# Performance work log

Measured on AMD Instinct MI355X. Metric: run time of the kernel, lower is better.

The kernel has to match this reference:

```python
import jax, jax.numpy as jnp
import numpy as np

MIN_EXP = 1    # log2(min_window=2)
MAX_EXP = 10   # log2(max_window=1024)
OUT_LEN = 16384  # reconstructed signal length L; encoded len = L*(1 - 2**-MAX_EXP)


def setup_inputs() -> dict:
    key = jax.random.key(0)
    k1, k2, k3 = jax.random.split(key, 3)
    B = 2048
    enc_len = OUT_LEN * (2 ** (1 - MIN_EXP)) - OUT_LEN // (2 ** MAX_EXP)  # 16368
    weights_len = 2 * (2 ** MAX_EXP) - 1  # 2047
    stdev = 1.0 / np.sqrt(weights_len)
    data = jax.random.normal(k1, (B, enc_len), dtype=jnp.float32)
    weights = jax.random.uniform(k2, (weights_len,), dtype=jnp.float32, minval=-stdev, maxval=stdev)
    bias = jax.random.uniform(k3, (MAX_EXP,), dtype=jnp.float32, minval=-stdev, maxval=stdev)
    return {"data": data, "weights": weights, "bias": bias}


def reference(data, weights, bias):
    """Transposed time-scale convolution: for each dyadic scale e (window w=2**e),
    the shared kernel weights[w-1:2w-1] is overlap-added (stride == window, so the
    windows tile the output exactly) scaled by that scale's coefficients, summed
    across scales, with a per-scale bias."""
    B = data.shape[0]
    out = jnp.zeros((B, OUT_LEN), dtype=data.dtype)
    offset = 0
    for e in range(MIN_EXP, MAX_EXP + 1):
        w = 2 ** e
        n = OUT_LEN // w                      # number of windows at this scale
        kern = weights[w - 1: 2 * w - 1]      # [w] kernel for this scale
        coeffs = data[:, offset: offset + n]  # [B, n]
        offset += n
        # transposed conv with stride = kernel size: outer product then tile
        contrib = (coeffs[:, :, None] * kern[None, None, :]).reshape(B, OUT_LEN)
        out = out + contrib + bias[e - 1]
    return out
```

## Files before the change

### kernel.cpp

```cpp
#include <hip/hip_runtime.h>
#include <hip/hip_bf16.h>

#define TSC_OUT_LEN 16384
#define TSC_ENC_LEN 16368

__global__ __launch_bounds__(256) void tsc_transpose_kernel(
    const float* __restrict__ data,
    const float* __restrict__ weights,
    const float* __restrict__ bias,
    float* __restrict__ out)
{
    __shared__ float wl[2048];
    const int tid = threadIdx.x;
    for (int i = tid; i < 2047; i += 256) wl[i + 1] = weights[i];
    if (tid == 0) wl[0] = 0.0f;
    __syncthreads();

    float bs = 0.0f;
#pragma unroll
    for (int i = 0; i < 10; ++i) bs += bias[i];

    const int b    = blockIdx.x >> 3;
    const int tile = (blockIdx.x & 7) << 11;
    const int j0   = tile + (tid << 3);
    const float* drow = data + (size_t)b * TSC_ENC_LEN;

    float acc[8];
#pragma unroll
    for (int k = 0; k < 8; ++k) acc[k] = bs;

    {
        const float4 d4 = *reinterpret_cast<const float4*>(drow + (j0 >> 1));
        const float w1 = wl[2], w2 = wl[3];
        acc[0] += d4.x * w1; acc[1] += d4.x * w2;
        acc[2] += d4.y * w1; acc[3] += d4.y * w2;
        acc[4] += d4.z * w1; acc[5] += d4.z * w2;
        acc[6] += d4.w * w1; acc[7] += d4.w * w2;
    }
    {
        const float2 d2 = *reinterpret_cast<const float2*>(drow + 8192 + (j0 >> 2));
        const float4 kv = *reinterpret_cast<const float4*>(&wl[4]);
        acc[0] += d2.x * kv.x; acc[1] += d2.x * kv.y;
        acc[2] += d2.x * kv.z; acc[3] += d2.x * kv.w;
        acc[4] += d2.y * kv.x; acc[5] += d2.y * kv.y;
        acc[6] += d2.y * kv.z; acc[7] += d2.y * kv.w;
    }
#pragma unroll
    for (int e = 3; e <= 10; ++e) {
        const int w   = 1 << e;
        const int off = TSC_OUT_LEN - (TSC_OUT_LEN >> (e - 1));
        const float c = drow[off + (j0 >> e)];
        const int  kb = w + (j0 & (w - 1));
        const float4 k0 = *reinterpret_cast<const float4*>(&wl[kb]);
        const float4 k1 = *reinterpret_cast<const float4*>(&wl[kb + 4]);
        acc[0] += c * k0.x; acc[1] += c * k0.y;
        acc[2] += c * k0.z; acc[3] += c * k0.w;
        acc[4] += c * k1.x; acc[5] += c * k1.y;
        acc[6] += c * k1.z; acc[7] += c * k1.w;
    }

    float4* o = reinterpret_cast<float4*>(out + (size_t)b * TSC_OUT_LEN + j0);
    o[0] = make_float4(acc[0], acc[1], acc[2], acc[3]);
    o[1] = make_float4(acc[4], acc[5], acc[6], acc[7]);
}

extern "C" void kernel_launch(void* const* d_in, const int* in_sizes, int n_in,
                              void* d_out, int out_size, void* d_ws, size_t ws_size,
                              hipStream_t stream) {
    const float* data    = (const float*)d_in[0];
    const float* weights = (const float*)d_in[1];
    const float* bias    = (const float*)d_in[2];
    float* out = (float*)d_out;

    const int B = in_sizes[0] / TSC_ENC_LEN;
    dim3 grid(B * 8);
    dim3 block(256);
    tsc_transpose_kernel<<<grid, block, 0, stream>>>(data, weights, bias, out);
}
```

Baseline: 238.9 us.

## Process eight rows per block with double-buffered loads and hoisted kernel weights

Each block now handles eight batch rows instead of one. Kernel weight slices are loaded from LDS into registers once per block, with the smallest scales broadcast via readfirstlane, and reused for every row. Loads for the next row are issued before the current row is computed, and outputs are written with nontemporal stores. This amortises the per-block LDS fill and bias reduction and overlaps memory latency, at the cost of more registers, a grid eight times smaller, and an assumption that B is divisible by eight.

```diff
diff --git a/kernel.cpp b/kernel.cpp
--- a/kernel.cpp
+++ b/kernel.cpp
@@ -1,8 +1,22 @@
 #include <hip/hip_runtime.h>
-#include <hip/hip_bf16.h>
 
 #define TSC_OUT_LEN 16384
 #define TSC_ENC_LEN 16368
+#define TSC_ROWS 8
+
+typedef float f32x4 __attribute__((ext_vector_type(4)));
+
+__device__ __forceinline__ float tsc_rfl(float x) {
+    return __uint_as_float(__builtin_amdgcn_readfirstlane(__float_as_uint(x)));
+}
+
+struct TscLd {
+    float4 d1;
+    float2 d2;
+    float  c3;
+    float  c4, c5, c6, c7, c8;
+    float  c9, c10;
+};
 
 __global__ __launch_bounds__(256) void tsc_transpose_kernel(
     const float* __restrict__ data,
@@ -13,55 +27,103 @@
     __shared__ float wl[2048];
     const int tid = threadIdx.x;
     for (int i = tid; i < 2047; i += 256) wl[i + 1] = weights[i];
-    if (tid == 0) wl[0] = 0.0f;
     __syncthreads();
+
+    const int tile = blockIdx.x & 7;
+    const int rg   = blockIdx.x >> 3;
+    const int j0   = (tile << 11) + (tid << 3);
 
     float bs = 0.0f;
 #pragma unroll
     for (int i = 0; i < 10; ++i) bs += bias[i];
 
-    const int b    = blockIdx.x >> 3;
-    const int tile = (blockIdx.x & 7) << 11;
-    const int j0   = tile + (tid << 3);
-    const float* drow = data + (size_t)b * TSC_ENC_LEN;
+    const float w1a = tsc_rfl(wl[2]), w1b = tsc_rfl(wl[3]);
+    const float w2a = tsc_rfl(wl[4]), w2b = tsc_rfl(wl[5]);
+    const float w2c = tsc_rfl(wl[6]), w2d = tsc_rfl(wl[7]);
+    float w3[8];
+#pragma unroll
+    for (int i = 0; i < 8; ++i) w3[i] = tsc_rfl(wl[8 + i]);
 
-    float acc[8];
+    float4 wa[7], wb[7];
 #pragma unroll
-    for (int k = 0; k < 8; ++k) acc[k] = bs;
-
-    {
-        const float4 d4 = *reinterpret_cast<const float4*>(drow + (j0 >> 1));
-        const float w1 = wl[2], w2 = wl[3];
-        acc[0] += d4.x * w1; acc[1] += d4.x * w2;
-        acc[2] += d4.y * w1; acc[3] += d4.y * w2;
-        acc[4] += d4.z * w1; acc[5] += d4.z * w2;
-        acc[6] += d4.w * w1; acc[7] += d4.w * w2;
-    }
-    {
-        const float2 d2 = *reinterpret_cast<const float2*>(drow + 8192 + (j0 >> 2));
-        const float4 kv = *reinterpret_cast<const float4*>(&wl[4]);
-        acc[0] += d2.x * kv.x; acc[1] += d2.x * kv.y;
-        acc[2] += d2.x * kv.z; acc[3] += d2.x * kv.w;
-        acc[4] += d2.y * kv.x; acc[5] += d2.y * kv.y;
-        acc[6] += d2.y * kv.z; acc[7] += d2.y * kv.w;
-    }
-#pragma unroll
-    for (int e = 3; e <= 10; ++e) {
-        const int w   = 1 << e;
-        const int off = TSC_OUT_LEN - (TSC_OUT_LEN >> (e - 1));
-        const float c = drow[off + (j0 >> e)];
-        const int  kb = w + (j0 & (w - 1));
-        const float4 k0 = *reinterpret_cast<const float4*>(&wl[kb]);
-        const float4 k1 = *reinterpret_cast<const float4*>(&wl[kb + 4]);
-        acc[0] += c * k0.x; acc[1] += c * k0.y;
-        acc[2] += c * k0.z; acc[3] += c * k0.w;
-        acc[4] += c * k1.x; acc[5] += c * k1.y;
-        acc[6] += c * k1.z; acc[7] += c * k1.w;
+    for (int e = 4; e <= 10; ++e) {
+        const int w  = 1 << e;
+        const int kb = w + (j0 & (w - 1));
+        wa[e - 4] = *reinterpret_cast<const float4*>(&wl[kb]);
+        wb[e - 4] = *reinterpret_cast<const float4*>(&wl[kb + 4]);
     }
 
-    float4* o = reinterpret_cast<float4*>(out + (size_t)b * TSC_OUT_LEN + j0);
-    o[0] = make_float4(acc[0], acc[1], acc[2], acc[3]);
-    o[1] = make_float4(acc[4], acc[5], acc[6], acc[7]);
+    const int i1 = (j0 >> 1);
+    const int i2 = 8192  + (j0 >> 2);
+    const int i3 = 12288 + (j0 >> 3);
+    const int i4 = 14336 + (j0 >> 4);
+    const int i5 = 15360 + (j0 >> 5);
+    const int i6 = 15872 + (j0 >> 6);
+    const int i7 = 16128 + (j0 >> 7);
+    const int i8 = 16256 + (j0 >> 8);
+    const int i9  = 16320 + __builtin_amdgcn_readfirstlane(j0 >> 9);
+    const int i10 = 16352 + __builtin_amdgcn_readfirstlane(j0 >> 10);
+
+    const float* drow = data + (size_t)rg * TSC_ROWS * TSC_ENC_LEN;
+    float*       orow = out  + (size_t)rg * TSC_ROWS * TSC_OUT_LEN + j0;
+
+    auto issue = [&](const float* dp, TscLd& L) {
+        L.d1  = *reinterpret_cast<const float4*>(dp + i1);
+        L.d2  = *reinterpret_cast<const float2*>(dp + i2);
+        L.c3  = dp[i3];
+        L.c4  = dp[i4];
+        L.c5  = dp[i5];
+        L.c6  = dp[i6];
+        L.c7  = dp[i7];
+        L.c8  = dp[i8];
+        L.c9  = dp[i9];
+        L.c10 = dp[i10];
+    };
+
+    auto compute_store = [&](const TscLd& L, float* op) {
+        float a0 = bs, a1 = bs, a2 = bs, a3 = bs;
+        float a4 = bs, a5 = bs, a6 = bs, a7 = bs;
+        a0 = fmaf(L.d1.x, w1a, a0); a1 = fmaf(L.d1.x, w1b, a1);
+        a2 = fmaf(L.d1.y, w1a, a2); a3 = fmaf(L.d1.y, w1b, a3);
+        a4 = fmaf(L.d1.z, w1a, a4); a5 = fmaf(L.d1.z, w1b, a5);
+        a6 = fmaf(L.d1.w, w1a, a6); a7 = fmaf(L.d1.w, w1b, a7);
+        a0 = fmaf(L.d2.x, w2a, a0); a1 = fmaf(L.d2.x, w2b, a1);
+        a2 = fmaf(L.d2.x, w2c, a2); a3 = fmaf(L.d2.x, w2d, a3);
+        a4 = fmaf(L.d2.y, w2a, a4); a5 = fmaf(L.d2.y, w2b, a5);
+        a6 = fmaf(L.d2.y, w2c, a6); a7 = fmaf(L.d2.y, w2d, a7);
+        a0 = fmaf(L.c3, w3[0], a0); a1 = fmaf(L.c3, w3[1], a1);
+        a2 = fmaf(L.c3, w3[2], a2); a3 = fmaf(L.c3, w3[3], a3);
+        a4 = fmaf(L.c3, w3[4], a4); a5 = fmaf(L.c3, w3[5], a5);
+        a6 = fmaf(L.c3, w3[6], a6); a7 = fmaf(L.c3, w3[7], a7);
+#define TSC_E(c, i) \
+        a0 = fmaf(c, wa[i].x, a0); a1 = fmaf(c, wa[i].y, a1); \
+        a2 = fmaf(c, wa[i].z, a2); a3 = fmaf(c, wa[i].w, a3); \
+        a4 = fmaf(c, wb[i].x, a4); a5 = fmaf(c, wb[i].y, a5); \
+        a6 = fmaf(c, wb[i].z, a6); a7 = fmaf(c, wb[i].w, a7);
+        TSC_E(L.c4, 0)
+        TSC_E(L.c5, 1)
+        TSC_E(L.c6, 2)
+        TSC_E(L.c7, 3)
+        TSC_E(L.c8, 4)
+        TSC_E(L.c9, 5)
+        TSC_E(L.c10, 6)
+#undef TSC_E
+        f32x4 v0 = {a0, a1, a2, a3};
+        f32x4 v1 = {a4, a5, a6, a7};
+        __builtin_nontemporal_store(v0, reinterpret_cast<f32x4*>(op));
+        __builtin_nontemporal_store(v1, reinterpret_cast<f32x4*>(op) + 1);
+    };
+
+    TscLd L0, L1;
+    issue(drow, L0);
+    for (int r = 0; r < TSC_ROWS; r += 2) {
+        issue(drow + TSC_ENC_LEN, L1);
+        compute_store(L0, orow);
+        if (r + 2 < TSC_ROWS) issue(drow + 2 * TSC_ENC_LEN, L0);
+        compute_store(L1, orow + TSC_OUT_LEN);
+        drow += 2 * TSC_ENC_LEN;
+        orow += 2 * TSC_OUT_LEN;
+    }
 }
 
 extern "C" void kernel_launch(void* const* d_in, const int* in_sizes, int n_in,
@@ -73,7 +135,7 @@
     float* out = (float*)d_out;
 
     const int B = in_sizes[0] / TSC_ENC_LEN;
-    dim3 grid(B * 8);
+    dim3 grid((B / TSC_ROWS) * 8);
     dim3 block(256);
     tsc_transpose_kernel<<<grid, block, 0, stream>>>(data, weights, bias, out);
 }
```

New measurement: 269.4 us. 12.8% more time.

## Stage per-row coefficients in LDS and loop over tiles with register-held kernel weights

Applied to the files above, without the earlier changes.

Each block now covers half an output row instead of an eighth. It first cooperatively loads all of that half's coefficients for every scale into shared memory with vectorised float4 loads. Kernel weights for each scale are hoisted into registers once, since each thread's offset within a window stays fixed across iterations, and the small-scale weights are made wave-uniform with readfirstlane. The aim is fewer scattered scalar global loads and less repeated weight fetching, in exchange for a larger LDS footprint, more registers, and fewer blocks.

```diff
diff --git a/kernel.cpp b/kernel.cpp
--- a/kernel.cpp
+++ b/kernel.cpp
@@ -1,67 +1,128 @@
 #include <hip/hip_runtime.h>
-#include <hip/hip_bf16.h>
 
 #define TSC_OUT_LEN 16384
 #define TSC_ENC_LEN 16368
 
-__global__ __launch_bounds__(256) void tsc_transpose_kernel(
+__device__ __forceinline__ float tsc_rfl(float x) {
+    return __uint_as_float(__builtin_amdgcn_readfirstlane(__float_as_uint(x)));
+}
+
+__global__ __launch_bounds__(256, 2) void tsc_transpose_kernel(
     const float* __restrict__ data,
     const float* __restrict__ weights,
     const float* __restrict__ bias,
     float* __restrict__ out)
 {
     __shared__ float wl[2048];
-    const int tid = threadIdx.x;
+    __shared__ __align__(16) float dL[8184];
+
+    const int tid  = threadIdx.x;
+    const int b    = blockIdx.x >> 1;
+    const int half = blockIdx.x & 1;
+    const float* drow = data + (size_t)b * TSC_ENC_LEN;
+
+    const float4* gaddr[8];
+#pragma unroll
+    for (int k = 0; k < 8; ++k) {
+        const int s = tid + (k << 8);
+        int e, base;
+        if      (s < 1024) { e = 1;  base = 0;    }
+        else if (s < 1536) { e = 2;  base = 1024; }
+        else if (s < 1792) { e = 3;  base = 1536; }
+        else if (s < 1920) { e = 4;  base = 1792; }
+        else if (s < 1984) { e = 5;  base = 1920; }
+        else if (s < 2016) { e = 6;  base = 1984; }
+        else if (s < 2032) { e = 7;  base = 2016; }
+        else if (s < 2040) { e = 8;  base = 2032; }
+        else if (s < 2044) { e = 9;  base = 2040; }
+        else               { e = 10; base = 2044; }
+        const int off_e  = TSC_OUT_LEN - (32768 >> e);
+        const int half_e = 8192 >> e;
+        gaddr[k] = reinterpret_cast<const float4*>(drow + off_e + half * half_e)
+                   + (s - base);
+    }
+    float4 sv[8];
+#pragma unroll
+    for (int k = 0; k < 8; ++k) {
+        const int s = tid + (k << 8);
+        if (s < 2046) sv[k] = *gaddr[k];
+    }
     for (int i = tid; i < 2047; i += 256) wl[i + 1] = weights[i];
-    if (tid == 0) wl[0] = 0.0f;
+#pragma unroll
+    for (int k = 0; k < 8; ++k) {
+        const int s = tid + (k << 8);
+        if (s < 2046) reinterpret_cast<float4*>(dL)[s] = sv[k];
+    }
     __syncthreads();
 
     float bs = 0.0f;
 #pragma unroll
     for (int i = 0; i < 10; ++i) bs += bias[i];
 
-    const int b    = blockIdx.x >> 3;
-    const int tile = (blockIdx.x & 7) << 11;
-    const int j0   = tile + (tid << 3);
-    const float* drow = data + (size_t)b * TSC_ENC_LEN;
+    const float w1a = tsc_rfl(wl[2]), w1b = tsc_rfl(wl[3]);
+    const float w2a = tsc_rfl(wl[4]), w2b = tsc_rfl(wl[5]);
+    const float w2c = tsc_rfl(wl[6]), w2d = tsc_rfl(wl[7]);
+    float w3[8];
+#pragma unroll
+    for (int i = 0; i < 8; ++i) w3[i] = tsc_rfl(wl[8 + i]);
 
-    float acc[8];
+    const int j8 = tid << 3;
+    float4 wa[7], wb[7];
 #pragma unroll
-    for (int k = 0; k < 8; ++k) acc[k] = bs;
-
-    {
-        const float4 d4 = *reinterpret_cast<const float4*>(drow + (j0 >> 1));
-        const float w1 = wl[2], w2 = wl[3];
-        acc[0] += d4.x * w1; acc[1] += d4.x * w2;
-        acc[2] += d4.y * w1; acc[3] += d4.y * w2;
-        acc[4] += d4.z * w1; acc[5] += d4.z * w2;
-        acc[6] += d4.w * w1; acc[7] += d4.w * w2;
-    }
-    {
-        const float2 d2 = *reinterpret_cast<const float2*>(drow + 8192 + (j0 >> 2));
-        const float4 kv = *reinterpret_cast<const float4*>(&wl[4]);
-        acc[0] += d2.x * kv.x; acc[1] += d2.x * kv.y;
-        acc[2] += d2.x * kv.z; acc[3] += d2.x * kv.w;
-        acc[4] += d2.y * kv.x; acc[5] += d2.y * kv.y;
-        acc[6] += d2.y * kv.z; acc[7] += d2.y * kv.w;
-    }
-#pragma unroll
-    for (int e = 3; e <= 10; ++e) {
-        const int w   = 1 << e;
-        const int off = TSC_OUT_LEN - (TSC_OUT_LEN >> (e - 1));
-        const float c = drow[off + (j0 >> e)];
-        const int  kb = w + (j0 & (w - 1));
-        const float4 k0 = *reinterpret_cast<const float4*>(&wl[kb]);
-        const float4 k1 = *reinterpret_cast<const float4*>(&wl[kb + 4]);
-        acc[0] += c * k0.x; acc[1] += c * k0.y;
-        acc[2] += c * k0.z; acc[3] += c * k0.w;
-        acc[4] += c * k1.x; acc[5] += c * k1.y;
-        acc[6] += c * k1.z; acc[7] += c * k1.w;
+    for (int e = 4; e <= 10; ++e) {
+        const int w  = 1 << e;
+        const int kb = w + (j8 & (w - 1));
+        wa[e - 4] = *reinterpret_cast<const float4*>(&wl[kb]);
+        wb[e - 4] = *reinterpret_cast<const float4*>(&wl[kb + 4]);
     }
 
-    float4* o = reinterpret_cast<float4*>(out + (size_t)b * TSC_OUT_LEN + j0);
-    o[0] = make_float4(acc[0], acc[1], acc[2], acc[3]);
-    o[1] = make_float4(acc[4], acc[5], acc[6], acc[7]);
+    float* orow = out + (size_t)b * TSC_OUT_LEN + (half << 13) + j8;
+
+#pragma unroll 2
+    for (int it = 0; it < 4; ++it) {
+        const int jl = (it << 11) + j8;
+        const float4 c1 = *reinterpret_cast<const float4*>(&dL[jl >> 1]);
+        const float2 c2 = *reinterpret_cast<const float2*>(&dL[4096 + (jl >> 2)]);
+        const float c3  = dL[6144 + (jl >> 3)];
+        const float c4  = dL[7168 + (jl >> 4)];
+        const float c5  = dL[7680 + (jl >> 5)];
+        const float c6  = dL[7936 + (jl >> 6)];
+        const float c7  = dL[8064 + (jl >> 7)];
+        const float c8  = dL[8128 + (jl >> 8)];
+        const float c9  = dL[8160 + (jl >> 9)];
+        const float c10 = dL[8176 + (jl >> 10)];
+
+        float a0 = bs, a1 = bs, a2 = bs, a3 = bs;
+        float a4 = bs, a5 = bs, a6 = bs, a7 = bs;
+        a0 = fmaf(c1.x, w1a, a0); a1 = fmaf(c1.x, w1b, a1);
+        a2 = fmaf(c1.y, w1a, a2); a3 = fmaf(c1.y, w1b, a3);
+        a4 = fmaf(c1.z, w1a, a4); a5 = fmaf(c1.z, w1b, a5);
+        a6 = fmaf(c1.w, w1a, a6); a7 = fmaf(c1.w, w1b, a7);
+        a0 = fmaf(c2.x, w2a, a0); a1 = fmaf(c2.x, w2b, a1);
+        a2 = fmaf(c2.x, w2c, a2); a3 = fmaf(c2.x, w2d, a3);
+        a4 = fmaf(c2.y, w2a, a4); a5 = fmaf(c2.y, w2b, a5);
+        a6 = fmaf(c2.y, w2c, a6); a7 = fmaf(c2.y, w2d, a7);
+        a0 = fmaf(c3, w3[0], a0); a1 = fmaf(c3, w3[1], a1);
+        a2 = fmaf(c3, w3[2], a2); a3 = fmaf(c3, w3[3], a3);
+        a4 = fmaf(c3, w3[4], a4); a5 = fmaf(c3, w3[5], a5);
+        a6 = fmaf(c3, w3[6], a6); a7 = fmaf(c3, w3[7], a7);
+#define TSC_E(c, i) \
+        a0 = fmaf(c, wa[i].x, a0); a1 = fmaf(c, wa[i].y, a1); \
+        a2 = fmaf(c, wa[i].z, a2); a3 = fmaf(c, wa[i].w, a3); \
+        a4 = fmaf(c, wb[i].x, a4); a5 = fmaf(c, wb[i].y, a5); \
+        a6 = fmaf(c, wb[i].z, a6); a7 = fmaf(c, wb[i].w, a7);
+        TSC_E(c4, 0)
+        TSC_E(c5, 1)
+        TSC_E(c6, 2)
+        TSC_E(c7, 3)
+        TSC_E(c8, 4)
+        TSC_E(c9, 5)
+        TSC_E(c10, 6)
+#undef TSC_E
+        float4* o4 = reinterpret_cast<float4*>(orow + (it << 11));
+        o4[0] = make_float4(a0, a1, a2, a3);
+        o4[1] = make_float4(a4, a5, a6, a7);
+    }
 }
 
 extern "C" void kernel_launch(void* const* d_in, const int* in_sizes, int n_in,
@@ -73,7 +134,7 @@
     float* out = (float*)d_out;
 
     const int B = in_sizes[0] / TSC_ENC_LEN;
-    dim3 grid(B * 8);
+    dim3 grid(B * 2);
     dim3 block(256);
     tsc_transpose_kernel<<<grid, block, 0, stream>>>(data, weights, bias, out);
 }
```

After: 276.9 us. 15.9% more time.

## Process four tiles per block with async LDS staging of coarse coefficients

Applied to the files above, without the earlier changes.

Each block now covers half a row (four 2048-element tiles) instead of one eighth. The per-block weight table load is therefore amortised over four times more output. Coefficients for scales 2 through 10 are staged into LDS via global_load_lds, while scale-1 coefficients are prefetched as float4 before the barrier. Weights are hoisted into registers, using readfirstlane for the uniform ones, and the FMAs are explicit. The trade-off is fewer blocks and more LDS and registers per block, which may reduce latency hiding.

```diff
diff --git a/kernel.cpp b/kernel.cpp
--- a/kernel.cpp
+++ b/kernel.cpp
@@ -1,67 +1,147 @@
 #include <hip/hip_runtime.h>
-#include <hip/hip_bf16.h>
 
 #define TSC_OUT_LEN 16384
 #define TSC_ENC_LEN 16368
 
-__global__ __launch_bounds__(256) void tsc_transpose_kernel(
+__device__ __forceinline__ float tsc_rfl(float x) {
+    return __uint_as_float(__builtin_amdgcn_readfirstlane(__float_as_uint(x)));
+}
+
+__global__ __launch_bounds__(256, 4) void tsc_transpose_kernel(
     const float* __restrict__ data,
     const float* __restrict__ weights,
     const float* __restrict__ bias,
     float* __restrict__ out)
 {
     __shared__ float wl[2048];
-    const int tid = threadIdx.x;
+    __shared__ __align__(16) float dL[4096];
+
+    const int tid  = threadIdx.x;
+    const int b    = blockIdx.x >> 1;
+    const int half = blockIdx.x & 1;
+    const float* drow = data + (size_t)b * TSC_ENC_LEN;
+
+    const int lane = tid & 63;
+    const int w_u  = __builtin_amdgcn_readfirstlane(tid >> 6);
+#pragma unroll
+    for (int k = 0; k < 4; ++k) {
+        const int cid = k + (w_u << 2);
+        const int s   = lane + (cid << 6);
+        int e, base;
+        if      (s < 512)  { e = 2;  base = 0;    }
+        else if (s < 768)  { e = 3;  base = 512;  }
+        else if (s < 896)  { e = 4;  base = 768;  }
+        else if (s < 960)  { e = 5;  base = 896;  }
+        else if (s < 992)  { e = 6;  base = 960;  }
+        else if (s < 1008) { e = 7;  base = 992;  }
+        else if (s < 1016) { e = 8;  base = 1008; }
+        else if (s < 1020) { e = 9;  base = 1016; }
+        else               { e = 10; base = 1020; }
+        const int off = TSC_OUT_LEN - (32768 >> e) + (half << (13 - e))
+                        + ((s - base) << 2);
+        const float* gs = (s < 1022) ? (drow + off) : drow;
+        __builtin_amdgcn_global_load_lds(
+            (const __attribute__((address_space(1))) unsigned int*)gs,
+            (__attribute__((address_space(3))) unsigned int*)(dL + (cid << 8)),
+            16, 0, 0);
+    }
+
+    const float* p1 = drow + (half << 12) + (tid << 2);
+    const float4 c1a = *reinterpret_cast<const float4*>(p1);
+    const float4 c1b = *reinterpret_cast<const float4*>(p1 + 1024);
+    const float4 c1c = *reinterpret_cast<const float4*>(p1 + 2048);
+    const float4 c1d = *reinterpret_cast<const float4*>(p1 + 3072);
+
     for (int i = tid; i < 2047; i += 256) wl[i + 1] = weights[i];
-    if (tid == 0) wl[0] = 0.0f;
-    __syncthreads();
 
     float bs = 0.0f;
 #pragma unroll
     for (int i = 0; i < 10; ++i) bs += bias[i];
 
-    const int b    = blockIdx.x >> 3;
-    const int tile = (blockIdx.x & 7) << 11;
-    const int j0   = tile + (tid << 3);
-    const float* drow = data + (size_t)b * TSC_ENC_LEN;
+    __syncthreads();
 
-    float acc[8];
+    const float w1a = tsc_rfl(wl[2]), w1b = tsc_rfl(wl[3]);
+    const float w2a = tsc_rfl(wl[4]), w2b = tsc_rfl(wl[5]);
+    const float w2c = tsc_rfl(wl[6]), w2d = tsc_rfl(wl[7]);
+    float w3[8];
 #pragma unroll
-    for (int k = 0; k < 8; ++k) acc[k] = bs;
+    for (int i = 0; i < 8; ++i) w3[i] = tsc_rfl(wl[8 + i]);
 
-    {
-        const float4 d4 = *reinterpret_cast<const float4*>(drow + (j0 >> 1));
-        const float w1 = wl[2], w2 = wl[3];
-        acc[0] += d4.x * w1; acc[1] += d4.x * w2;
-        acc[2] += d4.y * w1; acc[3] += d4.y * w2;
-        acc[4] += d4.z * w1; acc[5] += d4.z * w2;
-        acc[6] += d4.w * w1; acc[7] += d4.w * w2;
-    }
-    {
-        const float2 d2 = *reinterpret_cast<const float2*>(drow + 8192 + (j0 >> 2));
-        const float4 kv = *reinterpret_cast<const float4*>(&wl[4]);
-        acc[0] += d2.x * kv.x; acc[1] += d2.x * kv.y;
-        acc[2] += d2.x * kv.z; acc[3] += d2.x * kv.w;
-        acc[4] += d2.y * kv.x; acc[5] += d2.y * kv.y;
-        acc[6] += d2.y * kv.z; acc[7] += d2.y * kv.w;
-    }
+    const int j8 = tid << 3;
+    float4 wa[7], wb[7];
 #pragma unroll
-    for (int e = 3; e <= 10; ++e) {
-        const int w   = 1 << e;
-        const int off = TSC_OUT_LEN - (TSC_OUT_LEN >> (e - 1));
-        const float c = drow[off + (j0 >> e)];
-        const int  kb = w + (j0 & (w - 1));
-        const float4 k0 = *reinterpret_cast<const float4*>(&wl[kb]);
-        const float4 k1 = *reinterpret_cast<const float4*>(&wl[kb + 4]);
-        acc[0] += c * k0.x; acc[1] += c * k0.y;
-        acc[2] += c * k0.z; acc[3] += c * k0.w;
-        acc[4] += c * k1.x; acc[5] += c * k1.y;
-        acc[6] += c * k1.z; acc[7] += c * k1.w;
+    for (int e = 4; e <= 10; ++e) {
+        const int w  = 1 << e;
+        const int kb = w + (j8 & (w - 1));
+        wa[e - 4] = *reinterpret_cast<const float4*>(&wl[kb]);
+        wb[e - 4] = *reinterpret_cast<const float4*>(&wl[kb + 4]);
     }
 
-    float4* o = reinterpret_cast<float4*>(out + (size_t)b * TSC_OUT_LEN + j0);
-    o[0] = make_float4(acc[0], acc[1], acc[2], acc[3]);
-    o[1] = make_float4(acc[4], acc[5], acc[6], acc[7]);
+    float* orow = out + (size_t)b * TSC_OUT_LEN + (half << 13) + j8;
+
+#define TSC_ITER(IT, C1) do {                                              \
+        const int jl = ((IT) << 11) + j8;                                  \
+        const float2 c2 = *reinterpret_cast<const float2*>(&dL[jl >> 2]);  \
+        const float c3  = dL[2048 + (jl >> 3)];                            \
+        const float c4  = dL[3072 + (jl >> 4)];                            \
+        const float c5  = dL[3584 + (jl >> 5)];                            \
+        const float c6  = dL[3840 + (jl >> 6)];                            \
+        const float c7  = dL[3968 + (jl >> 7)];                            \
+        const float c8  = dL[4032 + (jl >> 8)];                            \
+        const float c9  = dL[4064 + (jl >> 9)];                            \
+        const float c10 = dL[4080 + (jl >> 10)];                           \
+        float a0 = bs, a1 = bs, a2 = bs, a3 = bs;                          \
+        float a4 = bs, a5 = bs, a6 = bs, a7 = bs;                          \
+        a0 = fmaf((C1).x, w1a, a0); a1 = fmaf((C1).x, w1b, a1);            \
+        a2 = fmaf((C1).y, w1a, a2); a3 = fmaf((C1).y, w1b, a3);            \
+        a4 = fmaf((C1).z, w1a, a4); a5 = fmaf((C1).z, w1b, a5);            \
+        a6 = fmaf((C1).w, w1a, a6); a7 = fmaf((C1).w, w1b, a7);            \
+        a0 = fmaf(c2.x, w2a, a0); a1 = fmaf(c2.x, w2b, a1);                \
+        a2 = fmaf(c2.x, w2c, a2); a3 = fmaf(c2.x, w2d, a3);                \
+        a4 = fmaf(c2.y, w2a, a4); a5 = fmaf(c2.y, w2b, a5);                \
+        a6 = fmaf(c2.y, w2c, a6); a7 = fmaf(c2.y, w2d, a7);                \
+        a0 = fmaf(c3, w3[0], a0); a1 = fmaf(c3, w3[1], a1);                \
+        a2 = fmaf(c3, w3[2], a2); a3 = fmaf(c3, w3[3], a3);                \
+        a4 = fmaf(c3, w3[4], a4); a5 = fmaf(c3, w3[5], a5);                \
+        a6 = fmaf(c3, w3[6], a6); a7 = fmaf(c3, w3[7], a7);                \
+        a0 = fmaf(c4, wa[0].x, a0); a1 = fmaf(c4, wa[0].y, a1);            \
+        a2 = fmaf(c4, wa[0].z, a2); a3 = fmaf(c4, wa[0].w, a3);            \
+        a4 = fmaf(c4, wb[0].x, a4); a5 = fmaf(c4, wb[0].y, a5);            \
+        a6 = fmaf(c4, wb[0].z, a6); a7 = fmaf(c4, wb[0].w, a7);            \
+        a0 = fmaf(c5, wa[1].x, a0); a1 = fmaf(c5, wa[1].y, a1);            \
+        a2 = fmaf(c5, wa[1].z, a2); a3 = fmaf(c5, wa[1].w, a3);            \
+        a4 = fmaf(c5, wb[1].x, a4); a5 = fmaf(c5, wb[1].y, a5);            \
+        a6 = fmaf(c5, wb[1].z, a6); a7 = fmaf(c5, wb[1].w, a7);            \
+        a0 = fmaf(c6, wa[2].x, a0); a1 = fmaf(c6, wa[2].y, a1);            \
+        a2 = fmaf(c6, wa[2].z, a2); a3 = fmaf(c6, wa[2].w, a3);            \
+        a4 = fmaf(c6, wb[2].x, a4); a5 = fmaf(c6, wb[2].y, a5);            \
+        a6 = fmaf(c6, wb[2].z, a6); a7 = fmaf(c6, wb[2].w, a7);            \
+        a0 = fmaf(c7, wa[3].x, a0); a1 = fmaf(c7, wa[3].y, a1);            \
+        a2 = fmaf(c7, wa[3].z, a2); a3 = fmaf(c7, wa[3].w, a3);            \
+        a4 = fmaf(c7, wb[3].x, a4); a5 = fmaf(c7, wb[3].y, a5);            \
+        a6 = fmaf(c7, wb[3].z, a6); a7 = fmaf(c7, wb[3].w, a7);            \
+        a0 = fmaf(c8, wa[4].x, a0); a1 = fmaf(c8, wa[4].y, a1);            \
+        a2 = fmaf(c8, wa[4].z, a2); a3 = fmaf(c8, wa[4].w, a3);            \
+        a4 = fmaf(c8, wb[4].x, a4); a5 = fmaf(c8, wb[4].y, a5);            \
+        a6 = fmaf(c8, wb[4].z, a6); a7 = fmaf(c8, wb[4].w, a7);            \
+        a0 = fmaf(c9, wa[5].x, a0); a1 = fmaf(c9, wa[5].y, a1);            \
+        a2 = fmaf(c9, wa[5].z, a2); a3 = fmaf(c9, wa[5].w, a3);            \
+        a4 = fmaf(c9, wb[5].x, a4); a5 = fmaf(c9, wb[5].y, a5);            \
+        a6 = fmaf(c9, wb[5].z, a6); a7 = fmaf(c9, wb[5].w, a7);            \
+        a0 = fmaf(c10, wa[6].x, a0); a1 = fmaf(c10, wa[6].y, a1);          \
+        a2 = fmaf(c10, wa[6].z, a2); a3 = fmaf(c10, wa[6].w, a3);          \
+        a4 = fmaf(c10, wb[6].x, a4); a5 = fmaf(c10, wb[6].y, a5);          \
+        a6 = fmaf(c10, wb[6].z, a6); a7 = fmaf(c10, wb[6].w, a7);          \
+        float4* o4 = reinterpret_cast<float4*>(orow + ((IT) << 11));       \
+        o4[0] = make_float4(a0, a1, a2, a3);                               \
+        o4[1] = make_float4(a4, a5, a6, a7);                               \
+    } while (0)
+
+    TSC_ITER(0, c1a);
+    TSC_ITER(1, c1b);
+    TSC_ITER(2, c1c);
+    TSC_ITER(3, c1d);
+#undef TSC_ITER
 }
 
 extern "C" void kernel_launch(void* const* d_in, const int* in_sizes, int n_in,
@@ -73,7 +153,7 @@
     float* out = (float*)d_out;
 
     const int B = in_sizes[0] / TSC_ENC_LEN;
-    dim3 grid(B * 8);
+    dim3 grid(B * 2);
     dim3 block(256);
     tsc_transpose_kernel<<<grid, block, 0, stream>>>(data, weights, bias, out);
 }
```

Result: no change. 241.4 us (+1.1%).
